# Optimization experiments

Measured on AMD Instinct MI355X. Metric: run time of the kernel, lower is better.

Reference implementation:

```python
import jax, jax.numpy as jnp
import numpy as np

_N = 2048          # matrix_size (A_sparse.shape[0] in the original)
_NNZ = 32768       # number of factor / pred entries
_LOGCOND_EPS = 1e-12


def setup_inputs() -> dict:
    key = jax.random.key(0)
    k1, k2, k3, k4, k5 = jax.random.split(key, 5)
    pred_values = jax.random.normal(k1, (_NNZ,), dtype=jnp.float32)
    active_scales = jax.random.uniform(k2, (_NNZ,), dtype=jnp.float32) * 0.05
    A_factor = jax.random.normal(k3, (_N, _N), dtype=jnp.float32)
    factor_rows = jax.random.randint(k4, (_NNZ,), 0, _N, dtype=jnp.int32)
    factor_cols = jax.random.randint(k5, (_NNZ,), 0, _N, dtype=jnp.int32)
    return {
        "pred_values": pred_values,
        "active_scales": active_scales,
        "A_factor": A_factor,
        "factor_rows": factor_rows,
        "factor_cols": factor_cols,
    }


def reference(pred_values, active_scales, A_factor, factor_rows, factor_cols):
    n = A_factor.shape[0]
    dt = pred_values.dtype
    # SPD system matrix A (stands in for the original fixed A_sparse)
    A = A_factor @ A_factor.T / jnp.asarray(n, dt) + jnp.eye(n, dtype=dt)
    # Sparse factor L assembled from predicted values (scatter-add, dup-safe),
    # unit diagonal keeps L A L^T well conditioned / SPD.
    L = jnp.eye(n, dtype=dt).at[factor_rows, factor_cols].add(pred_values * active_scales)
    # Preconditioned matrix M = L A L^T (symmetric PSD)
    M = L @ A @ L.T
    M = 0.5 * (M + M.T)
    evals = jnp.linalg.eigvalsh(M)  # ascending
    lam_min = jnp.maximum(evals[0], _LOGCOND_EPS)
    lam_max = jnp.maximum(evals[-1], _LOGCOND_EPS)
    # loss = log(lambda_max) - log(lambda_min) = log condition number
    return jnp.log(lam_max) - jnp.log(lam_min)
```

## Files before the change

kernel.cpp:

```cpp
#include <hip/hip_runtime.h>

#define N2 2048
#define NNZ 32768
#define LK 22
#define NBL 128
#define BINCAP 64

typedef __attribute__((ext_vector_type(8))) _Float16 half8;
typedef __attribute__((ext_vector_type(4))) float f32x4;

#define AGENT __HIP_MEMORY_SCOPE_AGENT
#define AS1C(p) ((const __attribute__((address_space(1))) unsigned int*)(p))
#define AS3(p)  ((__attribute__((address_space(3))) unsigned int*)(p))

__device__ __forceinline__ unsigned short f2h(float f) {
  _Float16 h = (_Float16)f;
  return *(unsigned short*)&h;
}
__device__ __forceinline__ float h2f(unsigned short u) {
  _Float16 h = *(_Float16*)&u;
  return (float)h;
}

__global__ __launch_bounds__(256) void convert_kernel(const float* __restrict__ W,
                                                      unsigned short* __restrict__ Hf,
                                                      unsigned* __restrict__ cnt) {
  if (blockIdx.x < 8) cnt[blockIdx.x * 256 + threadIdx.x] = 0;
  int i4 = blockIdx.x * 256 + threadIdx.x;
  float4 w = ((const float4*)W)[i4];
  ushort4 h;
  h.x = f2h(w.x); h.y = f2h(w.y); h.z = f2h(w.z); h.w = f2h(w.w);
  ((ushort4*)Hf)[i4] = h;
}

__device__ __forceinline__ void stage_tiles(const unsigned short* __restrict__ Hf,
                                            unsigned short* Xb, unsigned short* Yb,
                                            int row0, int col0, int kk,
                                            int srowX, int srowY, int scol, int wq) {
  __builtin_amdgcn_global_load_lds(
      AS1C(Hf + (size_t)(row0 + srowX) * 2048 + kk + scol),
      AS3(Xb + (wq * 16) * 32), 16, 0, 0);
#pragma unroll
  for (int q = 0; q < 2; ++q) {
    __builtin_amdgcn_global_load_lds(
        AS1C(Hf + (size_t)(col0 + srowY + q * 16) * 2048 + kk + scol),
        AS3(Yb + (wq * 32 + q * 16) * 32), 16, 0, 0);
  }
}

__global__ __launch_bounds__(512) void gemm_f16_kernel(const unsigned short* __restrict__ Hf,
                                                       unsigned short* __restrict__ Ah,
                                                       const float* __restrict__ pred,
                                                       const float* __restrict__ scal,
                                                       const int* __restrict__ rows,
                                                       const int* __restrict__ cols,
                                                       unsigned* __restrict__ cnt,
                                                       int* __restrict__ bcol,
                                                       float* __restrict__ bval) {
  const int tid = threadIdx.x;
  if (blockIdx.x < 64) {
    int k = blockIdx.x * 512 + tid;
    int r = rows[k];
    unsigned pos = atomicAdd(&cnt[r], 1u);
    if (pos < BINCAP) {
      bcol[r * BINCAP + pos] = cols[k];
      bval[r * BINCAP + pos] = pred[k] * scal[k];
    }
  }

  int bi, bj;
  bool diag;
  if (blockIdx.x < 32) {
    bi = blockIdx.x; bj = bi >> 1; diag = true;
  } else {
    int idx = blockIdx.x - 32;
    int j = 0;
    while (j < 14 && idx >= (j + 1) * (30 - j)) ++j;
    bj = j;
    bi = 2 * j + 2 + (idx - j * (31 - j));
    diag = false;
  }

  __shared__ __align__(16) char smem[49152];
  unsigned short* Xs = (unsigned short*)smem;
  unsigned short* Ys = (unsigned short*)(smem + 16384);
  float* Cred = (float*)smem;

  const int w = tid >> 6, lane = tid & 63;
  const int half = w >> 2, wq = w & 3;
  const int row0 = bi * 64, col0 = bj * 128;
  const int m0 = (wq & 1) * 32, n0 = (wq >> 1) * 64;
  f32x4 acc[2][4];
#pragma unroll
  for (int a = 0; a < 2; ++a)
#pragma unroll
    for (int b = 0; b < 4; ++b) acc[a][b] = (f32x4){0.f, 0.f, 0.f, 0.f};
  const int mrow = lane & 15, kseg = (lane >> 4) * 8;
  const int srowX = wq * 16 + (lane >> 2);
  const int srowY = wq * 32 + (lane >> 2);
  const int scol = (lane & 3) * 8;
  const int kbase = half * 1024;

  stage_tiles(Hf, Xs + (half * 2 + 0) * 2048, Ys + (half * 2 + 0) * 4096,
              row0, col0, kbase, srowX, srowY, scol, wq);

  for (int t = 0; t < 32; ++t) {
    const int cur = t & 1;
    __syncthreads();
    if (t < 31)
      stage_tiles(Hf, Xs + (half * 2 + (cur ^ 1)) * 2048,
                  Ys + (half * 2 + (cur ^ 1)) * 4096,
                  row0, col0, kbase + (t + 1) * 32, srowX, srowY, scol, wq);
    const unsigned short* Xb = Xs + (half * 2 + cur) * 2048;
    const unsigned short* Yb = Ys + (half * 2 + cur) * 4096;
    half8 af[2], bf[4];
#pragma unroll
    for (int q = 0; q < 2; ++q)
      af[q] = *(const half8*)(Xb + (m0 + q * 16 + mrow) * 32 + kseg);
#pragma unroll
    for (int q = 0; q < 4; ++q)
      bf[q] = *(const half8*)(Yb + (n0 + q * 16 + mrow) * 32 + kseg);
#pragma unroll
    for (int mt = 0; mt < 2; ++mt)
#pragma unroll
      for (int nt = 0; nt < 4; ++nt)
        acc[mt][nt] = __builtin_amdgcn_mfma_f32_16x16x32_f16(af[mt], bf[nt], acc[mt][nt], 0, 0, 0);
  }
  const int crow = (lane >> 4) * 4, ccol = lane & 15;
  __syncthreads();
  if (half == 1) {
#pragma unroll
    for (int mt = 0; mt < 2; ++mt)
#pragma unroll
      for (int nt = 0; nt < 4; ++nt)
#pragma unroll
        for (int r = 0; r < 4; ++r)
          Cred[(m0 + mt * 16 + crow + r) * 132 + n0 + nt * 16 + ccol] = acc[mt][nt][r];
  }
  __syncthreads();
  if (half == 0) {
    const float invn = 1.0f / 2048.0f;
#pragma unroll
    for (int mt = 0; mt < 2; ++mt)
#pragma unroll
      for (int nt = 0; nt < 4; ++nt) {
        const int gi0 = row0 + m0 + mt * 16 + crow;
        const int gj = col0 + n0 + nt * 16 + ccol;
        size_t base = (size_t)gi0 * 2048 + gj;
#pragma unroll
        for (int r = 0; r < 4; ++r) {
          const int li = (m0 + mt * 16 + crow + r) * 132 + n0 + nt * 16 + ccol;
          float val = (acc[mt][nt][r] + Cred[li]) * invn +
                      ((gi0 + r == gj) ? 1.0f : 0.0f);
          Ah[base + (size_t)r * 2048] = f2h(val);
          if (!diag) Cred[li] = val;
        }
      }
  }
  if (!diag) {
    __syncthreads();
    const int orow = tid >> 2;
    const int cseg = (tid & 3) * 16;
    unsigned short mv[16];
#pragma unroll
    for (int k = 0; k < 16; ++k)
      mv[k] = f2h(Cred[(cseg + k) * 132 + orow]);
    uint4* dst = (uint4*)(Ah + (size_t)(col0 + orow) * 2048 + row0 + cseg);
    dst[0] = *(uint4*)&mv[0];
    dst[1] = *(uint4*)&mv[8];
  }
}

__global__ __launch_bounds__(256) void gatherF_kernel(const unsigned* __restrict__ cnt,
                                                      const int* __restrict__ bcol,
                                                      const float* __restrict__ bval,
                                                      const unsigned short* __restrict__ Ah,
                                                      unsigned short* __restrict__ F) {
  const int r = blockIdx.x, tid = threadIdx.x;
  __shared__ int scol_[BINCAP];
  __shared__ float sval_[BINCAP];
  const unsigned ne = min(cnt[r], (unsigned)BINCAP);
  if (tid < ne) {
    scol_[tid] = bcol[r * BINCAP + tid];
    sval_[tid] = bval[r * BINCAP + tid];
  }
  __syncthreads();
  float acc[8] = {0.f, 0.f, 0.f, 0.f, 0.f, 0.f, 0.f, 0.f};
  unsigned e = 0;
  for (; e + 8 <= ne; e += 8) {
    uint4 q[8];
#pragma unroll
    for (int u = 0; u < 8; ++u)
      q[u] = *(const uint4*)(Ah + (size_t)scol_[e + u] * 2048 + tid * 8);
#pragma unroll
    for (int u = 0; u < 8; ++u) {
      half8 hv = *(half8*)&q[u];
      const float v = sval_[e + u];
#pragma unroll
      for (int k = 0; k < 8; ++k) acc[k] += v * (float)hv[k];
    }
  }
  for (; e + 4 <= ne; e += 4) {
    uint4 q[4];
#pragma unroll
    for (int u = 0; u < 4; ++u)
      q[u] = *(const uint4*)(Ah + (size_t)scol_[e + u] * 2048 + tid * 8);
#pragma unroll
    for (int u = 0; u < 4; ++u) {
      half8 hv = *(half8*)&q[u];
      const float v = sval_[e + u];
#pragma unroll
      for (int k = 0; k < 8; ++k) acc[k] += v * (float)hv[k];
    }
  }
  for (; e < ne; ++e) {
    uint4 qq = *(const uint4*)(Ah + (size_t)scol_[e] * 2048 + tid * 8);
    half8 hv = *(half8*)&qq;
    const float v = sval_[e];
#pragma unroll
    for (int k = 0; k < 8; ++k) acc[k] += v * (float)hv[k];
  }
  unsigned short o[8];
#pragma unroll
  for (int k = 0; k < 8; ++k) o[k] = f2h(acc[k]);
  *(uint4*)(F + (size_t)r * 2048 + tid * 8) = *(uint4*)o;
}

__global__ __launch_bounds__(256) void transpose_kernel(const unsigned short* __restrict__ F,
                                                        unsigned short* __restrict__ Ft) {
  __shared__ unsigned short T2[64][66];
  const int bi = blockIdx.x, bj = blockIdx.y;
  const int c8 = (threadIdx.x & 7) * 8;
  const int rr = threadIdx.x >> 3;
#pragma unroll
  for (int h = 0; h < 2; ++h) {
    const int r = rr + h * 32;
    uint4 raw = *(const uint4*)(F + (size_t)(bj * 64 + r) * 2048 + bi * 64 + c8);
    const unsigned* pw = (const unsigned*)&raw;
#pragma unroll
    for (int i = 0; i < 4; ++i)
      *(unsigned*)&T2[r][c8 + i * 2] = pw[i];
  }
  __syncthreads();
#pragma unroll
  for (int h = 0; h < 2; ++h) {
    const int r = rr + h * 32;
    unsigned short tv[8];
#pragma unroll
    for (int k = 0; k < 8; ++k) tv[k] = T2[c8 + k][r];
    *(uint4*)(Ft + (size_t)(bi * 64 + r) * 2048 + bj * 64 + c8) = *(uint4*)tv;
  }
}

__global__ __launch_bounds__(256) void finalM_kernel(const unsigned* __restrict__ cnt,
                                                     const int* __restrict__ bcol,
                                                     const float* __restrict__ bval,
                                                     const unsigned short* __restrict__ Ah,
                                                     const unsigned short* __restrict__ F,
                                                     const unsigned short* __restrict__ Ft,
                                                     float* __restrict__ M) {
  const int r = blockIdx.x, tid = threadIdx.x;
  __shared__ int scol_[BINCAP];
  __shared__ float sval_[BINCAP];
  const unsigned ne = min(cnt[r], (unsigned)BINCAP);
  if (tid < ne) {
    scol_[tid] = bcol[r * BINCAP + tid];
    sval_[tid] = bval[r * BINCAP + tid];
  }
  __syncthreads();
  float acc[8] = {0.f, 0.f, 0.f, 0.f, 0.f, 0.f, 0.f, 0.f};
  unsigned e = 0;
  for (; e + 8 <= ne; e += 8) {
    uint4 q[8];
#pragma unroll
    for (int u = 0; u < 8; ++u)
      q[u] = *(const uint4*)(Ft + (size_t)scol_[e + u] * 2048 + tid * 8);
#pragma unroll
    for (int u = 0; u < 8; ++u) {
      half8 hv = *(half8*)&q[u];
      const float v = sval_[e + u];
#pragma unroll
      for (int k = 0; k < 8; ++k) acc[k] += v * (float)hv[k];
    }
  }
  for (; e + 4 <= ne; e += 4) {
    uint4 q[4];
#pragma unroll
    for (int u = 0; u < 4; ++u)
      q[u] = *(const uint4*)(Ft + (size_t)scol_[e + u] * 2048 + tid * 8);
#pragma unroll
    for (int u = 0; u < 4; ++u) {
      half8 hv = *(half8*)&q[u];
      const float v = sval_[e + u];
#pragma unroll
      for (int k = 0; k < 8; ++k) acc[k] += v * (float)hv[k];
    }
  }
  for (; e < ne; ++e) {
    uint4 qq = *(const uint4*)(Ft + (size_t)scol_[e] * 2048 + tid * 8);
    half8 hv = *(half8*)&qq;
    const float v = sval_[e];
#pragma unroll
    for (int k = 0; k < 8; ++k) acc[k] += v * (float)hv[k];
  }
  const size_t off = (size_t)r * 2048 + tid * 8;
  uint4 ra = *(const uint4*)(Ah + off);
  uint4 rf = *(const uint4*)(F + off);
  uint4 rt = *(const uint4*)(Ft + off);
  half8 ha = *(half8*)&ra, hf = *(half8*)&rf, ht = *(half8*)&rt;
  float out[8];
#pragma unroll
  for (int k = 0; k < 8; ++k)
    out[k] = (float)ha[k] + ((float)hf[k] + (float)ht[k]) + acc[k];
  float4* Mo = (float4*)(M + off);
  Mo[0] = (float4){out[0], out[1], out[2], out[3]};
  Mo[1] = (float4){out[4], out[5], out[6], out[7]};
}

__device__ __forceinline__ float block_sum8(float v, float* red) {
#pragma unroll
  for (int off = 32; off; off >>= 1) v += __shfl_down(v, off);
  if ((threadIdx.x & 63) == 0) red[threadIdx.x >> 6] = v;
  __syncthreads();
  float r = ((red[0] + red[1]) + (red[2] + red[3])) +
            ((red[4] + red[5]) + (red[6] + red[7]));
  __syncthreads();
  return r;
}

__global__ __launch_bounds__(512) void lanczos_kernel(const float* __restrict__ M,
                                                      unsigned long long* __restrict__ Z0,
                                                      unsigned long long* __restrict__ Z1,
                                                      float* __restrict__ out) {
  const int tid = threadIdx.x, b = blockIdx.x;
  const int wave = tid >> 6, lane = tid & 63;
  __shared__ __align__(16) float Mlds[16 * 2048];
  __shared__ __align__(16) float VA[2048];
  __shared__ __align__(16) float VB[2048];
  __shared__ float red[8];
  __shared__ float al[LK + 2], b2[LK + 2];
  __shared__ float bnds[2], res[2];

  const float* Mblk = M + (size_t)b * 16 * 2048;
#pragma unroll
  for (int q = 0; q < 16; ++q)
    __builtin_amdgcn_global_load_lds(AS1C(Mblk + wave * 4096 + q * 256 + lane * 4),
                                     AS3(Mlds + wave * 4096 + q * 256), 16, 0, 0);

  float pv[4];
  float part = 0.f;
#pragma unroll
  for (int t = 0; t < 4; ++t) {
    int i = t * 512 + tid;
    unsigned u = (unsigned)i * 2654435761u;
    u ^= u >> 16; u *= 2246822519u; u ^= u >> 13;
    float rv = (float)(u >> 8) * (2.f / 16777216.f) - 1.f;
    pv[t] = rv;
    part += rv * rv;
  }
  float nrm = block_sum8(part, red);
  float innm = rsqrtf(nrm);
#pragma unroll
  for (int t = 0; t < 4; ++t) {
    int i = t * 512 + tid;
    VA[i] = pv[t] * innm;
    VB[i] = 0.f;
  }
  __syncthreads();

  float* Vcur = VA;
  float* Vprev = VB;
  float beta_prev = 0.f;

  for (int j = 1; j <= LK; ++j) {
    unsigned long long* Z = (j & 1) ? Z0 : Z1;
#pragma unroll
    for (int rr = 0; rr < 2; ++rr) {
      const int r = b * 16 + wave * 2 + rr;
      const float4* Mr = (const float4*)(Mlds + (wave * 2 + rr) * 2048);
      float s = 0.f;
#pragma unroll
      for (int t = 0; t < 8; ++t) {
        int idx = t * 64 + lane;
        float4 m4 = Mr[idx];
        float4 v4 = ((const float4*)Vcur)[idx];
        s += m4.x * v4.x + m4.y * v4.y + m4.z * v4.z + m4.w * v4.w;
      }
#pragma unroll
      for (int off = 32; off; off >>= 1) s += __shfl_down(s, off);
      if (lane == 0) {
        float zv = s - beta_prev * Vprev[r];
        unsigned long long pk = ((unsigned long long)(unsigned)j << 32) |
                                (unsigned long long)(unsigned)__float_as_uint(zv);
        __hip_atomic_store(&Z[r], pk, __ATOMIC_RELAXED, AGENT);
      }
    }

    float va[4];
#pragma unroll
    for (int t = 0; t < 4; ++t) va[t] = Vcur[t * 512 + tid];

    unsigned long long w4[4];
    int rounds = 0;
    for (;;) {
      bool ok = true;
#pragma unroll
      for (int t = 0; t < 4; ++t) {
        w4[t] = __hip_atomic_load(&Z[t * 512 + tid], __ATOMIC_RELAXED, AGENT);
        ok &= ((unsigned)(w4[t] >> 32) == (unsigned)j);
      }
      if (ok) break;
      if (rounds == 1)      __builtin_amdgcn_s_sleep(1);
      else if (rounds == 2) __builtin_amdgcn_s_sleep(2);
      else if (rounds >= 3) __builtin_amdgcn_s_sleep(8);
      ++rounds;
    }
    float za[4];
    float pa = 0.f;
#pragma unroll
    for (int t = 0; t < 4; ++t) {
      za[t] = __uint_as_float((unsigned)w4[t]);
      pa += za[t] * va[t];
    }
    float alpha = block_sum8(pa, red);
    float pb = 0.f;
#pragma unroll
    for (int t = 0; t < 4; ++t) {
      float rsd = za[t] - alpha * va[t];
      pb += rsd * rsd;
    }
    float beta2 = block_sum8(pb, red);
    float beta = sqrtf(fmaxf(beta2, 1e-30f));
    float invb = 1.f / beta;
    if (tid == 0) { al[j] = alpha; b2[j] = beta2; }
#pragma unroll
    for (int t = 0; t < 4; ++t) {
      int i = t * 512 + tid;
      Vprev[i] = (za[t] - alpha * va[t]) * invb;
    }
    float* tmp = Vprev; Vprev = Vcur; Vcur = tmp;
    beta_prev = beta;
    __syncthreads();
  }

  if (b == 0) {
    if (tid == 0) {
      float lo = 1e30f, hi = -1e30f;
      for (int i = 1; i <= LK; ++i) {
        float bl = (i > 1) ? sqrtf(b2[i - 1]) : 0.f;
        float br = (i < LK) ? sqrtf(b2[i]) : 0.f;
        lo = fminf(lo, al[i] - bl - br);
        hi = fmaxf(hi, al[i] + bl + br);
      }
      bnds[0] = lo; bnds[1] = hi;
    }
    __syncthreads();
    if (wave < 2) {
      const int tcount = (wave == 0) ? 1 : LK;
      float lo = bnds[0], hi = bnds[1];
      for (int round = 0; round < 4; ++round) {
        float x = lo + (hi - lo) * (float)(lane + 1) * (1.f / 65.f);
        int cnt = 0;
        float d = al[1] - x;
        if (fabsf(d) < 1e-25f) d = -1e-25f;
        if (d < 0.f) cnt++;
        for (int i = 2; i <= LK; ++i) {
          d = (al[i] - x) - b2[i - 1] / d;
          if (fabsf(d) < 1e-25f) d = -1e-25f;
          if (d < 0.f) cnt++;
        }
        bool ab = (cnt >= tcount);
        float cand_hi = ab ? x : hi;
        float cand_lo = ab ? lo : x;
#pragma unroll
        for (int off = 32; off; off >>= 1) {
          cand_hi = fminf(cand_hi, __shfl_down(cand_hi, off));
          cand_lo = fmaxf(cand_lo, __shfl_down(cand_lo, off));
        }
        cand_hi = __shfl(cand_hi, 0);
        cand_lo = __shfl(cand_lo, 0);
        hi = cand_hi;
        lo = fminf(cand_lo, hi);
      }
      if (lane == 0) res[wave] = 0.5f * (lo + hi);
    }
    __syncthreads();
    if (tid == 0) {
      float lmin = fmaxf(res[0], 1e-12f);
      float lmax = fmaxf(res[1], 1e-12f);
      out[0] = logf(lmax) - logf(lmin);
    }
  }
}

extern "C" void kernel_launch(void* const* d_in, const int* in_sizes, int n_in,
                              void* d_out, int out_size, void* d_ws, size_t ws_size,
                              hipStream_t stream) {
  const float* pred = (const float*)d_in[0];
  const float* scal = (const float*)d_in[1];
  const float* W    = (const float*)d_in[2];
  const int*   rows = (const int*)d_in[3];
  const int*   cols = (const int*)d_in[4];
  float* out = (float*)d_out;

  char* ws = (char*)d_ws;
  const size_t MB = 1024 * 1024;
  unsigned short* Hf = (unsigned short*)(ws);
  unsigned short* Ah = (unsigned short*)(ws + 8 * MB);
  unsigned short* F  = (unsigned short*)(ws + 16 * MB);
  unsigned short* Ft = (unsigned short*)(ws);
  float* M = (float*)(ws + 24 * MB);
  char* ctrl = ws + 40 * MB;
  unsigned* cnt  = (unsigned*)(ctrl);
  int*      bcol = (int*)(ctrl + 8192);
  float*    bval = (float*)(ctrl + 8192 + 524288);
  unsigned long long* Z0 = (unsigned long long*)(ctrl + 8192 + 1048576);
  unsigned long long* Z1 = (unsigned long long*)(ctrl + 8192 + 1048576 + 16384);

  convert_kernel<<<4096, 256, 0, stream>>>(W, Hf, cnt);
  gemm_f16_kernel<<<272, 512, 0, stream>>>(Hf, Ah, pred, scal, rows, cols, cnt, bcol, bval);

  gatherF_kernel<<<2048, 256, 0, stream>>>(cnt, bcol, bval, Ah, F);
  transpose_kernel<<<dim3(32, 32), 256, 0, stream>>>(F, Ft);
  finalM_kernel<<<2048, 256, 0, stream>>>(cnt, bcol, bval, Ah, F, Ft, M);

  lanczos_kernel<<<NBL, 512, 0, stream>>>(M, Z0, Z1, out);
}
```

Baseline: 251.2 us.

## Replace sparse row-gather products with dense fp16 MFMA GEMMs on scattered S

```diff
diff --git a/kernel.cpp b/kernel.cpp
--- a/kernel.cpp
+++ b/kernel.cpp
@@ -4,7 +4,6 @@
 #define NNZ 32768
 #define LK 22
 #define NBL 128
-#define BINCAP 64
 
 typedef __attribute__((ext_vector_type(8))) _Float16 half8;
 typedef __attribute__((ext_vector_type(4))) float f32x4;
@@ -24,27 +23,78 @@
 
 __global__ __launch_bounds__(256) void convert_kernel(const float* __restrict__ W,
                                                       unsigned short* __restrict__ Hf,
-                                                      unsigned* __restrict__ cnt) {
-  if (blockIdx.x < 8) cnt[blockIdx.x * 256 + threadIdx.x] = 0;
+                                                      float* __restrict__ Sf) {
   int i4 = blockIdx.x * 256 + threadIdx.x;
+  ((float4*)Sf)[i4] = (float4){0.f, 0.f, 0.f, 0.f};
   float4 w = ((const float4*)W)[i4];
   ushort4 h;
   h.x = f2h(w.x); h.y = f2h(w.y); h.z = f2h(w.z); h.w = f2h(w.w);
   ((ushort4*)Hf)[i4] = h;
 }
 
-__device__ __forceinline__ void stage_tiles(const unsigned short* __restrict__ Hf,
-                                            unsigned short* Xb, unsigned short* Yb,
-                                            int row0, int col0, int kk,
-                                            int srowX, int srowY, int scol, int wq) {
+__global__ __launch_bounds__(256) void cvtS_kernel(const float* __restrict__ Sf,
+                                                   unsigned short* __restrict__ Sh) {
+  int i4 = blockIdx.x * 256 + threadIdx.x;
+  float4 s = ((const float4*)Sf)[i4];
+  ushort4 h;
+  h.x = f2h(s.x); h.y = f2h(s.y); h.z = f2h(s.z); h.w = f2h(s.w);
+  ((ushort4*)Sh)[i4] = h;
+}
+
+__device__ __forceinline__ void stage_tiles2(const unsigned short* __restrict__ X,
+                                             const unsigned short* __restrict__ Y,
+                                             unsigned short* Xb, unsigned short* Yb,
+                                             int row0, int col0, int kk,
+                                             int srowX, int srowY, int scol, int wq) {
   __builtin_amdgcn_global_load_lds(
-      AS1C(Hf + (size_t)(row0 + srowX) * 2048 + kk + scol),
+      AS1C(X + (size_t)(row0 + srowX) * 2048 + kk + scol),
       AS3(Xb + (wq * 16) * 32), 16, 0, 0);
 #pragma unroll
   for (int q = 0; q < 2; ++q) {
     __builtin_amdgcn_global_load_lds(
-        AS1C(Hf + (size_t)(col0 + srowY + q * 16) * 2048 + kk + scol),
+        AS1C(Y + (size_t)(col0 + srowY + q * 16) * 2048 + kk + scol),
         AS3(Yb + (wq * 32 + q * 16) * 32), 16, 0, 0);
+  }
+}
+
+__device__ __forceinline__ void gemm_core(const unsigned short* __restrict__ X,
+                                          const unsigned short* __restrict__ Y,
+                                          char* smem, int tid, int row0, int col0,
+                                          f32x4 acc[2][4]) {
+  unsigned short* Xs = (unsigned short*)smem;
+  unsigned short* Ys = (unsigned short*)(smem + 16384);
+  const int w = tid >> 6, lane = tid & 63;
+  const int half = w >> 2, wq = w & 3;
+  const int m0 = (wq & 1) * 32, n0 = (wq >> 1) * 64;
+  const int mrow = lane & 15, kseg = (lane >> 4) * 8;
+  const int srowX = wq * 16 + (lane >> 2);
+  const int srowY = wq * 32 + (lane >> 2);
+  const int scol = (lane & 3) * 8;
+  const int kbase = half * 1024;
+
+  stage_tiles2(X, Y, Xs + (half * 2 + 0) * 2048, Ys + (half * 2 + 0) * 4096,
+               row0, col0, kbase, srowX, srowY, scol, wq);
+  for (int t = 0; t < 32; ++t) {
+    const int cur = t & 1;
+    __syncthreads();
+    if (t < 31)
+      stage_tiles2(X, Y, Xs + (half * 2 + (cur ^ 1)) * 2048,
+                   Ys + (half * 2 + (cur ^ 1)) * 4096,
+                   row0, col0, kbase + (t + 1) * 32, srowX, srowY, scol, wq);
+    const unsigned short* Xb = Xs + (half * 2 + cur) * 2048;
+    const unsigned short* Yb = Ys + (half * 2 + cur) * 4096;
+    half8 af[2], bf[4];
+#pragma unroll
+    for (int q = 0; q < 2; ++q)
+      af[q] = *(const half8*)(Xb + (m0 + q * 16 + mrow) * 32 + kseg);
+#pragma unroll
+    for (int q = 0; q < 4; ++q)
+      bf[q] = *(const half8*)(Yb + (n0 + q * 16 + mrow) * 32 + kseg);
+#pragma unroll
+    for (int mt = 0; mt < 2; ++mt)
+#pragma unroll
+      for (int nt = 0; nt < 4; ++nt)
+        acc[mt][nt] = __builtin_amdgcn_mfma_f32_16x16x32_f16(af[mt], bf[nt], acc[mt][nt], 0, 0, 0);
   }
 }
 
@@ -54,18 +104,11 @@
                                                        const float* __restrict__ scal,
                                                        const int* __restrict__ rows,
                                                        const int* __restrict__ cols,
-                                                       unsigned* __restrict__ cnt,
-                                                       int* __restrict__ bcol,
-                                                       float* __restrict__ bval) {
+                                                       float* __restrict__ Sf) {
   const int tid = threadIdx.x;
   if (blockIdx.x < 64) {
     int k = blockIdx.x * 512 + tid;
-    int r = rows[k];
-    unsigned pos = atomicAdd(&cnt[r], 1u);
-    if (pos < BINCAP) {
-      bcol[r * BINCAP + pos] = cols[k];
-      bval[r * BINCAP + pos] = pred[k] * scal[k];
-    }
+    atomicAdd(&Sf[(size_t)rows[k] * 2048 + cols[k]], pred[k] * scal[k]);
   }
 
   int bi, bj;
@@ -82,10 +125,7 @@
   }
 
   __shared__ __align__(16) char smem[49152];
-  unsigned short* Xs = (unsigned short*)smem;
-  unsigned short* Ys = (unsigned short*)(smem + 16384);
   float* Cred = (float*)smem;
-
   const int w = tid >> 6, lane = tid & 63;
   const int half = w >> 2, wq = w & 3;
   const int row0 = bi * 64, col0 = bj * 128;
@@ -95,37 +135,9 @@
   for (int a = 0; a < 2; ++a)
 #pragma unroll
     for (int b = 0; b < 4; ++b) acc[a][b] = (f32x4){0.f, 0.f, 0.f, 0.f};
-  const int mrow = lane & 15, kseg = (lane >> 4) * 8;
-  const int srowX = wq * 16 + (lane >> 2);
-  const int srowY = wq * 32 + (lane >> 2);
-  const int scol = (lane & 3) * 8;
-  const int kbase = half * 1024;
-
-  stage_tiles(Hf, Xs + (half * 2 + 0) * 2048, Ys + (half * 2 + 0) * 4096,
-              row0, col0, kbase, srowX, srowY, scol, wq);
-
-  for (int t = 0; t < 32; ++t) {
-    const int cur = t & 1;
-    __syncthreads();
-    if (t < 31)
-      stage_tiles(Hf, Xs + (half * 2 + (cur ^ 1)) * 2048,
-                  Ys + (half * 2 + (cur ^ 1)) * 4096,
-                  row0, col0, kbase + (t + 1) * 32, srowX, srowY, scol, wq);
-    const unsigned short* Xb = Xs + (half * 2 + cur) * 2048;
-    const unsigned short* Yb = Ys + (half * 2 + cur) * 4096;
-    half8 af[2], bf[4];
-#pragma unroll
-    for (int q = 0; q < 2; ++q)
-      af[q] = *(const half8*)(Xb + (m0 + q * 16 + mrow) * 32 + kseg);
-#pragma unroll
-    for (int q = 0; q < 4; ++q)
-      bf[q] = *(const half8*)(Yb + (n0 + q * 16 + mrow) * 32 + kseg);
-#pragma unroll
-    for (int mt = 0; mt < 2; ++mt)
-#pragma unroll
-      for (int nt = 0; nt < 4; ++nt)
-        acc[mt][nt] = __builtin_amdgcn_mfma_f32_16x16x32_f16(af[mt], bf[nt], acc[mt][nt], 0, 0, 0);
-  }
+
+  gemm_core(Hf, Hf, smem, tid, row0, col0, acc);
+
   const int crow = (lane >> 4) * 4, ccol = lane & 15;
   __syncthreads();
   if (half == 1) {
@@ -171,59 +183,52 @@
   }
 }
 
-__global__ __launch_bounds__(256) void gatherF_kernel(const unsigned* __restrict__ cnt,
-                                                      const int* __restrict__ bcol,
-                                                      const float* __restrict__ bval,
-                                                      const unsigned short* __restrict__ Ah,
-                                                      unsigned short* __restrict__ F) {
-  const int r = blockIdx.x, tid = threadIdx.x;
-  __shared__ int scol_[BINCAP];
-  __shared__ float sval_[BINCAP];
-  const unsigned ne = min(cnt[r], (unsigned)BINCAP);
-  if (tid < ne) {
-    scol_[tid] = bcol[r * BINCAP + tid];
-    sval_[tid] = bval[r * BINCAP + tid];
-  }
-  __syncthreads();
-  float acc[8] = {0.f, 0.f, 0.f, 0.f, 0.f, 0.f, 0.f, 0.f};
-  unsigned e = 0;
-  for (; e + 8 <= ne; e += 8) {
-    uint4 q[8];
-#pragma unroll
-    for (int u = 0; u < 8; ++u)
-      q[u] = *(const uint4*)(Ah + (size_t)scol_[e + u] * 2048 + tid * 8);
-#pragma unroll
-    for (int u = 0; u < 8; ++u) {
-      half8 hv = *(half8*)&q[u];
-      const float v = sval_[e + u];
-#pragma unroll
-      for (int k = 0; k < 8; ++k) acc[k] += v * (float)hv[k];
-    }
-  }
-  for (; e + 4 <= ne; e += 4) {
-    uint4 q[4];
-#pragma unroll
-    for (int u = 0; u < 4; ++u)
-      q[u] = *(const uint4*)(Ah + (size_t)scol_[e + u] * 2048 + tid * 8);
-#pragma unroll
-    for (int u = 0; u < 4; ++u) {
-      half8 hv = *(half8*)&q[u];
-      const float v = sval_[e + u];
-#pragma unroll
-      for (int k = 0; k < 8; ++k) acc[k] += v * (float)hv[k];
-    }
-  }
-  for (; e < ne; ++e) {
-    uint4 qq = *(const uint4*)(Ah + (size_t)scol_[e] * 2048 + tid * 8);
-    half8 hv = *(half8*)&qq;
-    const float v = sval_[e];
-#pragma unroll
-    for (int k = 0; k < 8; ++k) acc[k] += v * (float)hv[k];
-  }
-  unsigned short o[8];
-#pragma unroll
-  for (int k = 0; k < 8; ++k) o[k] = f2h(acc[k]);
-  *(uint4*)(F + (size_t)r * 2048 + tid * 8) = *(uint4*)o;
+__global__ __launch_bounds__(512) void gemmSA_kernel(const unsigned short* __restrict__ Sh,
+                                                     const unsigned short* __restrict__ Ah,
+                                                     unsigned short* __restrict__ F) {
+  const int tid = threadIdx.x;
+  const int bi = blockIdx.x >> 4, bj = blockIdx.x & 15;
+  __shared__ __align__(16) char smem[49152];
+  float* Cred = (float*)smem;
+  const int w = tid >> 6, lane = tid & 63;
+  const int half = w >> 2, wq = w & 3;
+  const int row0 = bi * 64, col0 = bj * 128;
+  const int m0 = (wq & 1) * 32, n0 = (wq >> 1) * 64;
+  f32x4 acc[2][4];
+#pragma unroll
+  for (int a = 0; a < 2; ++a)
+#pragma unroll
+    for (int b = 0; b < 4; ++b) acc[a][b] = (f32x4){0.f, 0.f, 0.f, 0.f};
+
+  gemm_core(Sh, Ah, smem, tid, row0, col0, acc);
+
+  const int crow = (lane >> 4) * 4, ccol = lane & 15;
+  __syncthreads();
+  if (half == 1) {
+#pragma unroll
+    for (int mt = 0; mt < 2; ++mt)
+#pragma unroll
+      for (int nt = 0; nt < 4; ++nt)
+#pragma unroll
+        for (int r = 0; r < 4; ++r)
+          Cred[(m0 + mt * 16 + crow + r) * 132 + n0 + nt * 16 + ccol] = acc[mt][nt][r];
+  }
+  __syncthreads();
+  if (half == 0) {
+#pragma unroll
+    for (int mt = 0; mt < 2; ++mt)
+#pragma unroll
+      for (int nt = 0; nt < 4; ++nt) {
+        const int gi0 = row0 + m0 + mt * 16 + crow;
+        const int gj = col0 + n0 + nt * 16 + ccol;
+        size_t base = (size_t)gi0 * 2048 + gj;
+#pragma unroll
+        for (int r = 0; r < 4; ++r) {
+          const int li = (m0 + mt * 16 + crow + r) * 132 + n0 + nt * 16 + ccol;
+          F[base + (size_t)r * 2048] = f2h(acc[mt][nt][r] + Cred[li]);
+        }
+      }
+  }
 }
 
 __global__ __launch_bounds__(256) void transpose_kernel(const unsigned short* __restrict__ F,
@@ -252,69 +257,56 @@
   }
 }
 
-__global__ __launch_bounds__(256) void finalM_kernel(const unsigned* __restrict__ cnt,
-                                                     const int* __restrict__ bcol,
-                                                     const float* __restrict__ bval,
+__global__ __launch_bounds__(512) void gemmSM_kernel(const unsigned short* __restrict__ Sh,
+                                                     const unsigned short* __restrict__ Fy,
                                                      const unsigned short* __restrict__ Ah,
-                                                     const unsigned short* __restrict__ F,
                                                      const unsigned short* __restrict__ Ft,
                                                      float* __restrict__ M) {
-  const int r = blockIdx.x, tid = threadIdx.x;
-  __shared__ int scol_[BINCAP];
-  __shared__ float sval_[BINCAP];
-  const unsigned ne = min(cnt[r], (unsigned)BINCAP);
-  if (tid < ne) {
-    scol_[tid] = bcol[r * BINCAP + tid];
-    sval_[tid] = bval[r * BINCAP + tid];
-  }
-  __syncthreads();
-  float acc[8] = {0.f, 0.f, 0.f, 0.f, 0.f, 0.f, 0.f, 0.f};
-  unsigned e = 0;
-  for (; e + 8 <= ne; e += 8) {
-    uint4 q[8];
-#pragma unroll
-    for (int u = 0; u < 8; ++u)
-      q[u] = *(const uint4*)(Ft + (size_t)scol_[e + u] * 2048 + tid * 8);
-#pragma unroll
-    for (int u = 0; u < 8; ++u) {
-      half8 hv = *(half8*)&q[u];
-      const float v = sval_[e + u];
-#pragma unroll
-      for (int k = 0; k < 8; ++k) acc[k] += v * (float)hv[k];
-    }
-  }
-  for (; e + 4 <= ne; e += 4) {
-    uint4 q[4];
-#pragma unroll
-    for (int u = 0; u < 4; ++u)
-      q[u] = *(const uint4*)(Ft + (size_t)scol_[e + u] * 2048 + tid * 8);
-#pragma unroll
-    for (int u = 0; u < 4; ++u) {
-      half8 hv = *(half8*)&q[u];
-      const float v = sval_[e + u];
-#pragma unroll
-      for (int k = 0; k < 8; ++k) acc[k] += v * (float)hv[k];
-    }
-  }
-  for (; e < ne; ++e) {
-    uint4 qq = *(const uint4*)(Ft + (size_t)scol_[e] * 2048 + tid * 8);
-    half8 hv = *(half8*)&qq;
-    const float v = sval_[e];
-#pragma unroll
-    for (int k = 0; k < 8; ++k) acc[k] += v * (float)hv[k];
-  }
-  const size_t off = (size_t)r * 2048 + tid * 8;
-  uint4 ra = *(const uint4*)(Ah + off);
-  uint4 rf = *(const uint4*)(F + off);
-  uint4 rt = *(const uint4*)(Ft + off);
-  half8 ha = *(half8*)&ra, hf = *(half8*)&rf, ht = *(half8*)&rt;
-  float out[8];
-#pragma unroll
-  for (int k = 0; k < 8; ++k)
-    out[k] = (float)ha[k] + ((float)hf[k] + (float)ht[k]) + acc[k];
-  float4* Mo = (float4*)(M + off);
-  Mo[0] = (float4){out[0], out[1], out[2], out[3]};
-  Mo[1] = (float4){out[4], out[5], out[6], out[7]};
+  const int tid = threadIdx.x;
+  const int bi = blockIdx.x >> 4, bj = blockIdx.x & 15;
+  __shared__ __align__(16) char smem[49152];
+  float* Cred = (float*)smem;
+  const int w = tid >> 6, lane = tid & 63;
+  const int half = w >> 2, wq = w & 3;
+  const int row0 = bi * 64, col0 = bj * 128;
+  const int m0 = (wq & 1) * 32, n0 = (wq >> 1) * 64;
+  f32x4 acc[2][4];
+#pragma unroll
+  for (int a = 0; a < 2; ++a)
+#pragma unroll
+    for (int b = 0; b < 4; ++b) acc[a][b] = (f32x4){0.f, 0.f, 0.f, 0.f};
+
+  gemm_core(Sh, Fy, smem, tid, row0, col0, acc);
+
+  const int crow = (lane >> 4) * 4, ccol = lane & 15;
+  __syncthreads();
+  if (half == 1) {
+#pragma unroll
+    for (int mt = 0; mt < 2; ++mt)
+#pragma unroll
+      for (int nt = 0; nt < 4; ++nt)
+#pragma unroll
+        for (int r = 0; r < 4; ++r)
+          Cred[(m0 + mt * 16 + crow + r) * 132 + n0 + nt * 16 + ccol] = acc[mt][nt][r];
+  }
+  __syncthreads();
+  if (half == 0) {
+#pragma unroll
+    for (int mt = 0; mt < 2; ++mt)
+#pragma unroll
+      for (int nt = 0; nt < 4; ++nt) {
+        const int gi0 = row0 + m0 + mt * 16 + crow;
+        const int gj = col0 + n0 + nt * 16 + ccol;
+        size_t base = (size_t)gi0 * 2048 + gj;
+#pragma unroll
+        for (int r = 0; r < 4; ++r) {
+          const size_t off = base + (size_t)r * 2048;
+          const int li = (m0 + mt * 16 + crow + r) * 132 + n0 + nt * 16 + ccol;
+          float sft = acc[mt][nt][r] + Cred[li];
+          M[off] = h2f(Ah[off]) + (h2f(Fy[off]) + h2f(Ft[off])) + sft;
+        }
+      }
+  }
 }
 
 __device__ __forceinline__ float block_sum8(float v, float* red) {
@@ -506,23 +498,21 @@
   char* ws = (char*)d_ws;
   const size_t MB = 1024 * 1024;
   unsigned short* Hf = (unsigned short*)(ws);
+  unsigned short* Sh = (unsigned short*)(ws);
   unsigned short* Ah = (unsigned short*)(ws + 8 * MB);
   unsigned short* F  = (unsigned short*)(ws + 16 * MB);
-  unsigned short* Ft = (unsigned short*)(ws);
-  float* M = (float*)(ws + 24 * MB);
-  char* ctrl = ws + 40 * MB;
-  unsigned* cnt  = (unsigned*)(ctrl);
-  int*      bcol = (int*)(ctrl + 8192);
-  float*    bval = (float*)(ctrl + 8192 + 524288);
-  unsigned long long* Z0 = (unsigned long long*)(ctrl + 8192 + 1048576);
-  unsigned long long* Z1 = (unsigned long long*)(ctrl + 8192 + 1048576 + 16384);
-
-  convert_kernel<<<4096, 256, 0, stream>>>(W, Hf, cnt);
-  gemm_f16_kernel<<<272, 512, 0, stream>>>(Hf, Ah, pred, scal, rows, cols, cnt, bcol, bval);
-
-  gatherF_kernel<<<2048, 256, 0, stream>>>(cnt, bcol, bval, Ah, F);
+  float* Sf = (float*)(ws + 24 * MB);
+  float* M  = (float*)(ws + 24 * MB);
+  unsigned short* Ft = (unsigned short*)(ws + 40 * MB);
+  unsigned long long* Z0 = (unsigned long long*)(ws + 48 * MB);
+  unsigned long long* Z1 = (unsigned long long*)(ws + 48 * MB + 16384);
+
+  convert_kernel<<<4096, 256, 0, stream>>>(W, Hf, Sf);
+  gemm_f16_kernel<<<272, 512, 0, stream>>>(Hf, Ah, pred, scal, rows, cols, Sf);
+  cvtS_kernel<<<4096, 256, 0, stream>>>(Sf, Sh);
+  gemmSA_kernel<<<512, 512, 0, stream>>>(Sh, Ah, F);
   transpose_kernel<<<dim3(32, 32), 256, 0, stream>>>(F, Ft);
-  finalM_kernel<<<2048, 256, 0, stream>>>(cnt, bcol, bval, Ah, F, Ft, M);
+  gemmSM_kernel<<<512, 512, 0, stream>>>(Sh, F, Ah, Ft, M);
 
   lanczos_kernel<<<NBL, 512, 0, stream>>>(M, Z0, Z1, out);
 }
```

Result: slower. 284.5 us (+13.3%).

## Rewrite L A L^T as (LW)(LW)^T/n plus sparse L L^T

Applied to the files above, without the earlier changes.

```diff
diff --git a/kernel.cpp b/kernel.cpp
--- a/kernel.cpp
+++ b/kernel.cpp
@@ -22,10 +22,13 @@
   return (float)h;
 }
 
+
 __global__ __launch_bounds__(256) void convert_kernel(const float* __restrict__ W,
                                                       unsigned short* __restrict__ Hf,
-                                                      unsigned* __restrict__ cnt) {
-  if (blockIdx.x < 8) cnt[blockIdx.x * 256 + threadIdx.x] = 0;
+                                                      unsigned* __restrict__ cntR,
+                                                      unsigned* __restrict__ cntC) {
+  if (blockIdx.x < 8)       cntR[blockIdx.x * 256 + threadIdx.x] = 0;
+  else if (blockIdx.x < 16) cntC[(blockIdx.x - 8) * 256 + threadIdx.x] = 0;
   int i4 = blockIdx.x * 256 + threadIdx.x;
   float4 w = ((const float4*)W)[i4];
   ushort4 h;
@@ -33,41 +36,102 @@
   ((ushort4*)Hf)[i4] = h;
 }
 
-__device__ __forceinline__ void stage_tiles(const unsigned short* __restrict__ Hf,
-                                            unsigned short* Xb, unsigned short* Yb,
-                                            int row0, int col0, int kk,
-                                            int srowX, int srowY, int scol, int wq) {
+__global__ __launch_bounds__(256) void fill_kernel(const float* __restrict__ pred,
+                                                   const float* __restrict__ scal,
+                                                   const int* __restrict__ rows,
+                                                   const int* __restrict__ cols,
+                                                   unsigned* __restrict__ cntR,
+                                                   int* __restrict__ binRc,
+                                                   float* __restrict__ binRv,
+                                                   unsigned* __restrict__ cntC,
+                                                   int* __restrict__ binCr,
+                                                   float* __restrict__ binCv) {
+  int k = blockIdx.x * 256 + threadIdx.x;
+  int r = rows[k], c = cols[k];
+  float v = pred[k] * scal[k];
+  unsigned pR = atomicAdd(&cntR[r], 1u);
+  if (pR < BINCAP) { binRc[r * BINCAP + pR] = c; binRv[r * BINCAP + pR] = v; }
+  unsigned pC = atomicAdd(&cntC[c], 1u);
+  if (pC < BINCAP) { binCr[c * BINCAP + pC] = r; binCv[c * BINCAP + pC] = v; }
+}
+
+__global__ __launch_bounds__(256) void gatherG_kernel(const unsigned* __restrict__ cntR,
+                                                      const int* __restrict__ binRc,
+                                                      const float* __restrict__ binRv,
+                                                      const unsigned short* __restrict__ Hf,
+                                                      unsigned short* __restrict__ Gh) {
+  const int r = blockIdx.x, tid = threadIdx.x;
+  __shared__ int scol_[BINCAP];
+  __shared__ float sval_[BINCAP];
+  const unsigned ne = min(cntR[r], (unsigned)BINCAP);
+  if (tid < ne) {
+    scol_[tid] = binRc[r * BINCAP + tid];
+    sval_[tid] = binRv[r * BINCAP + tid];
+  }
+  __syncthreads();
+  uint4 own = *(const uint4*)(Hf + (size_t)r * 2048 + tid * 8);
+  half8 ho = *(half8*)&own;
+  float acc[8];
+#pragma unroll
+  for (int k = 0; k < 8; ++k) acc[k] = (float)ho[k];
+  unsigned e = 0;
+  for (; e + 8 <= ne; e += 8) {
+    uint4 q[8];
+#pragma unroll
+    for (int u = 0; u < 8; ++u)
+      q[u] = *(const uint4*)(Hf + (size_t)scol_[e + u] * 2048 + tid * 8);
+#pragma unroll
+    for (int u = 0; u < 8; ++u) {
+      half8 hv = *(half8*)&q[u];
+      const float v = sval_[e + u];
+#pragma unroll
+      for (int k = 0; k < 8; ++k) acc[k] += v * (float)hv[k];
+    }
+  }
+  for (; e + 4 <= ne; e += 4) {
+    uint4 q[4];
+#pragma unroll
+    for (int u = 0; u < 4; ++u)
+      q[u] = *(const uint4*)(Hf + (size_t)scol_[e + u] * 2048 + tid * 8);
+#pragma unroll
+    for (int u = 0; u < 4; ++u) {
+      half8 hv = *(half8*)&q[u];
+      const float v = sval_[e + u];
+#pragma unroll
+      for (int k = 0; k < 8; ++k) acc[k] += v * (float)hv[k];
+    }
+  }
+  for (; e < ne; ++e) {
+    uint4 qq = *(const uint4*)(Hf + (size_t)scol_[e] * 2048 + tid * 8);
+    half8 hv = *(half8*)&qq;
+    const float v = sval_[e];
+#pragma unroll
+    for (int k = 0; k < 8; ++k) acc[k] += v * (float)hv[k];
+  }
+  unsigned short o[8];
+#pragma unroll
+  for (int k = 0; k < 8; ++k) o[k] = f2h(acc[k]);
+  *(uint4*)(Gh + (size_t)r * 2048 + tid * 8) = *(uint4*)o;
+}
+
+__device__ __forceinline__ void stage_tiles2(const unsigned short* __restrict__ X,
+                                             unsigned short* Xb, unsigned short* Yb,
+                                             int row0, int col0, int kk,
+                                             int srowX, int srowY, int scol, int wq) {
   __builtin_amdgcn_global_load_lds(
-      AS1C(Hf + (size_t)(row0 + srowX) * 2048 + kk + scol),
+      AS1C(X + (size_t)(row0 + srowX) * 2048 + kk + scol),
       AS3(Xb + (wq * 16) * 32), 16, 0, 0);
 #pragma unroll
   for (int q = 0; q < 2; ++q) {
     __builtin_amdgcn_global_load_lds(
-        AS1C(Hf + (size_t)(col0 + srowY + q * 16) * 2048 + kk + scol),
+        AS1C(X + (size_t)(col0 + srowY + q * 16) * 2048 + kk + scol),
         AS3(Yb + (wq * 32 + q * 16) * 32), 16, 0, 0);
   }
 }
 
-__global__ __launch_bounds__(512) void gemm_f16_kernel(const unsigned short* __restrict__ Hf,
-                                                       unsigned short* __restrict__ Ah,
-                                                       const float* __restrict__ pred,
-                                                       const float* __restrict__ scal,
-                                                       const int* __restrict__ rows,
-                                                       const int* __restrict__ cols,
-                                                       unsigned* __restrict__ cnt,
-                                                       int* __restrict__ bcol,
-                                                       float* __restrict__ bval) {
+__global__ __launch_bounds__(512) void gemmM_kernel(const unsigned short* __restrict__ Gh,
+                                                    float* __restrict__ M) {
   const int tid = threadIdx.x;
-  if (blockIdx.x < 64) {
-    int k = blockIdx.x * 512 + tid;
-    int r = rows[k];
-    unsigned pos = atomicAdd(&cnt[r], 1u);
-    if (pos < BINCAP) {
-      bcol[r * BINCAP + pos] = cols[k];
-      bval[r * BINCAP + pos] = pred[k] * scal[k];
-    }
-  }
-
   int bi, bj;
   bool diag;
   if (blockIdx.x < 32) {
@@ -101,16 +165,15 @@
   const int scol = (lane & 3) * 8;
   const int kbase = half * 1024;
 
-  stage_tiles(Hf, Xs + (half * 2 + 0) * 2048, Ys + (half * 2 + 0) * 4096,
-              row0, col0, kbase, srowX, srowY, scol, wq);
-
+  stage_tiles2(Gh, Xs + (half * 2 + 0) * 2048, Ys + (half * 2 + 0) * 4096,
+               row0, col0, kbase, srowX, srowY, scol, wq);
   for (int t = 0; t < 32; ++t) {
     const int cur = t & 1;
     __syncthreads();
     if (t < 31)
-      stage_tiles(Hf, Xs + (half * 2 + (cur ^ 1)) * 2048,
-                  Ys + (half * 2 + (cur ^ 1)) * 4096,
-                  row0, col0, kbase + (t + 1) * 32, srowX, srowY, scol, wq);
+      stage_tiles2(Gh, Xs + (half * 2 + (cur ^ 1)) * 2048,
+                   Ys + (half * 2 + (cur ^ 1)) * 4096,
+                   row0, col0, kbase + (t + 1) * 32, srowX, srowY, scol, wq);
     const unsigned short* Xb = Xs + (half * 2 + cur) * 2048;
     const unsigned short* Yb = Ys + (half * 2 + cur) * 4096;
     half8 af[2], bf[4];
@@ -152,7 +215,7 @@
           const int li = (m0 + mt * 16 + crow + r) * 132 + n0 + nt * 16 + ccol;
           float val = (acc[mt][nt][r] + Cred[li]) * invn +
                       ((gi0 + r == gj) ? 1.0f : 0.0f);
-          Ah[base + (size_t)r * 2048] = f2h(val);
+          M[base + (size_t)r * 2048] = val;
           if (!diag) Cred[li] = val;
         }
       }
@@ -161,160 +224,49 @@
     __syncthreads();
     const int orow = tid >> 2;
     const int cseg = (tid & 3) * 16;
-    unsigned short mv[16];
+    float mv[16];
 #pragma unroll
     for (int k = 0; k < 16; ++k)
-      mv[k] = f2h(Cred[(cseg + k) * 132 + orow]);
-    uint4* dst = (uint4*)(Ah + (size_t)(col0 + orow) * 2048 + row0 + cseg);
-    dst[0] = *(uint4*)&mv[0];
-    dst[1] = *(uint4*)&mv[8];
-  }
-}
-
-__global__ __launch_bounds__(256) void gatherF_kernel(const unsigned* __restrict__ cnt,
-                                                      const int* __restrict__ bcol,
-                                                      const float* __restrict__ bval,
-                                                      const unsigned short* __restrict__ Ah,
-                                                      unsigned short* __restrict__ F) {
-  const int r = blockIdx.x, tid = threadIdx.x;
-  __shared__ int scol_[BINCAP];
-  __shared__ float sval_[BINCAP];
-  const unsigned ne = min(cnt[r], (unsigned)BINCAP);
-  if (tid < ne) {
-    scol_[tid] = bcol[r * BINCAP + tid];
-    sval_[tid] = bval[r * BINCAP + tid];
-  }
-  __syncthreads();
-  float acc[8] = {0.f, 0.f, 0.f, 0.f, 0.f, 0.f, 0.f, 0.f};
-  unsigned e = 0;
-  for (; e + 8 <= ne; e += 8) {
-    uint4 q[8];
-#pragma unroll
-    for (int u = 0; u < 8; ++u)
-      q[u] = *(const uint4*)(Ah + (size_t)scol_[e + u] * 2048 + tid * 8);
-#pragma unroll
-    for (int u = 0; u < 8; ++u) {
-      half8 hv = *(half8*)&q[u];
-      const float v = sval_[e + u];
-#pragma unroll
-      for (int k = 0; k < 8; ++k) acc[k] += v * (float)hv[k];
-    }
-  }
-  for (; e + 4 <= ne; e += 4) {
-    uint4 q[4];
-#pragma unroll
-    for (int u = 0; u < 4; ++u)
-      q[u] = *(const uint4*)(Ah + (size_t)scol_[e + u] * 2048 + tid * 8);
-#pragma unroll
-    for (int u = 0; u < 4; ++u) {
-      half8 hv = *(half8*)&q[u];
-      const float v = sval_[e + u];
-#pragma unroll
-      for (int k = 0; k < 8; ++k) acc[k] += v * (float)hv[k];
-    }
-  }
-  for (; e < ne; ++e) {
-    uint4 qq = *(const uint4*)(Ah + (size_t)scol_[e] * 2048 + tid * 8);
-    half8 hv = *(half8*)&qq;
-    const float v = sval_[e];
-#pragma unroll
-    for (int k = 0; k < 8; ++k) acc[k] += v * (float)hv[k];
-  }
-  unsigned short o[8];
-#pragma unroll
-  for (int k = 0; k < 8; ++k) o[k] = f2h(acc[k]);
-  *(uint4*)(F + (size_t)r * 2048 + tid * 8) = *(uint4*)o;
-}
-
-__global__ __launch_bounds__(256) void transpose_kernel(const unsigned short* __restrict__ F,
-                                                        unsigned short* __restrict__ Ft) {
-  __shared__ unsigned short T2[64][66];
-  const int bi = blockIdx.x, bj = blockIdx.y;
-  const int c8 = (threadIdx.x & 7) * 8;
-  const int rr = threadIdx.x >> 3;
-#pragma unroll
-  for (int h = 0; h < 2; ++h) {
-    const int r = rr + h * 32;
-    uint4 raw = *(const uint4*)(F + (size_t)(bj * 64 + r) * 2048 + bi * 64 + c8);
-    const unsigned* pw = (const unsigned*)&raw;
-#pragma unroll
-    for (int i = 0; i < 4; ++i)
-      *(unsigned*)&T2[r][c8 + i * 2] = pw[i];
-  }
-  __syncthreads();
-#pragma unroll
-  for (int h = 0; h < 2; ++h) {
-    const int r = rr + h * 32;
-    unsigned short tv[8];
-#pragma unroll
-    for (int k = 0; k < 8; ++k) tv[k] = T2[c8 + k][r];
-    *(uint4*)(Ft + (size_t)(bi * 64 + r) * 2048 + bj * 64 + c8) = *(uint4*)tv;
-  }
-}
-
-__global__ __launch_bounds__(256) void finalM_kernel(const unsigned* __restrict__ cnt,
-                                                     const int* __restrict__ bcol,
-                                                     const float* __restrict__ bval,
-                                                     const unsigned short* __restrict__ Ah,
-                                                     const unsigned short* __restrict__ F,
-                                                     const unsigned short* __restrict__ Ft,
-                                                     float* __restrict__ M) {
-  const int r = blockIdx.x, tid = threadIdx.x;
-  __shared__ int scol_[BINCAP];
-  __shared__ float sval_[BINCAP];
-  const unsigned ne = min(cnt[r], (unsigned)BINCAP);
-  if (tid < ne) {
-    scol_[tid] = bcol[r * BINCAP + tid];
-    sval_[tid] = bval[r * BINCAP + tid];
-  }
-  __syncthreads();
-  float acc[8] = {0.f, 0.f, 0.f, 0.f, 0.f, 0.f, 0.f, 0.f};
-  unsigned e = 0;
-  for (; e + 8 <= ne; e += 8) {
-    uint4 q[8];
-#pragma unroll
-    for (int u = 0; u < 8; ++u)
-      q[u] = *(const uint4*)(Ft + (size_t)scol_[e + u] * 2048 + tid * 8);
-#pragma unroll
-    for (int u = 0; u < 8; ++u) {
-      half8 hv = *(half8*)&q[u];
-      const float v = sval_[e + u];
-#pragma unroll
-      for (int k = 0; k < 8; ++k) acc[k] += v * (float)hv[k];
-    }
-  }
-  for (; e + 4 <= ne; e += 4) {
-    uint4 q[4];
-#pragma unroll
-    for (int u = 0; u < 4; ++u)
-      q[u] = *(const uint4*)(Ft + (size_t)scol_[e + u] * 2048 + tid * 8);
-#pragma unroll
-    for (int u = 0; u < 4; ++u) {
-      half8 hv = *(half8*)&q[u];
-      const float v = sval_[e + u];
-#pragma unroll
-      for (int k = 0; k < 8; ++k) acc[k] += v * (float)hv[k];
-    }
-  }
-  for (; e < ne; ++e) {
-    uint4 qq = *(const uint4*)(Ft + (size_t)scol_[e] * 2048 + tid * 8);
-    half8 hv = *(half8*)&qq;
-    const float v = sval_[e];
-#pragma unroll
-    for (int k = 0; k < 8; ++k) acc[k] += v * (float)hv[k];
-  }
-  const size_t off = (size_t)r * 2048 + tid * 8;
-  uint4 ra = *(const uint4*)(Ah + off);
-  uint4 rf = *(const uint4*)(F + off);
-  uint4 rt = *(const uint4*)(Ft + off);
-  half8 ha = *(half8*)&ra, hf = *(half8*)&rf, ht = *(half8*)&rt;
-  float out[8];
-#pragma unroll
-  for (int k = 0; k < 8; ++k)
-    out[k] = (float)ha[k] + ((float)hf[k] + (float)ht[k]) + acc[k];
-  float4* Mo = (float4*)(M + off);
-  Mo[0] = (float4){out[0], out[1], out[2], out[3]};
-  Mo[1] = (float4){out[4], out[5], out[6], out[7]};
+      mv[k] = Cred[(cseg + k) * 132 + orow];
+    float4* dst = (float4*)(M + (size_t)(col0 + orow) * 2048 + row0 + cseg);
+    dst[0] = (float4){mv[0], mv[1], mv[2], mv[3]};
+    dst[1] = (float4){mv[4], mv[5], mv[6], mv[7]};
+    dst[2] = (float4){mv[8], mv[9], mv[10], mv[11]};
+    dst[3] = (float4){mv[12], mv[13], mv[14], mv[15]};
+  }
+}
+
+__global__ __launch_bounds__(256) void scatterS_kernel(const float* __restrict__ pred,
+                                                       const float* __restrict__ scal,
+                                                       const int* __restrict__ rows,
+                                                       const int* __restrict__ cols,
+                                                       const unsigned* __restrict__ cntC,
+                                                       const int* __restrict__ binCr,
+                                                       const float* __restrict__ binCv,
+                                                       float* __restrict__ M) {
+  const int tid = threadIdx.x;
+  if (blockIdx.x < 128) {
+    int k = blockIdx.x * 256 + tid;
+    int r = rows[k], c = cols[k];
+    float v = pred[k] * scal[k];
+    atomicAdd(&M[(size_t)r * 2048 + c], v);
+    atomicAdd(&M[(size_t)c * 2048 + r], v);
+    return;
+  }
+  const int c = blockIdx.x - 128;
+  __shared__ int rr_[BINCAP];
+  __shared__ float vv_[BINCAP];
+  const unsigned nc = min(cntC[c], (unsigned)BINCAP);
+  if (tid < nc) {
+    rr_[tid] = binCr[c * BINCAP + tid];
+    vv_[tid] = binCv[c * BINCAP + tid];
+  }
+  __syncthreads();
+  const unsigned np = nc * nc;
+  for (unsigned p = tid; p < np; p += 256) {
+    unsigned i1 = p / nc, i2 = p - i1 * nc;
+    atomicAdd(&M[(size_t)rr_[i1] * 2048 + rr_[i2]], vv_[i1] * vv_[i2]);
+  }
 }
 
 __device__ __forceinline__ float block_sum8(float v, float* red) {
@@ -506,23 +458,25 @@
   char* ws = (char*)d_ws;
   const size_t MB = 1024 * 1024;
   unsigned short* Hf = (unsigned short*)(ws);
-  unsigned short* Ah = (unsigned short*)(ws + 8 * MB);
-  unsigned short* F  = (unsigned short*)(ws + 16 * MB);
-  unsigned short* Ft = (unsigned short*)(ws);
-  float* M = (float*)(ws + 24 * MB);
-  char* ctrl = ws + 40 * MB;
-  unsigned* cnt  = (unsigned*)(ctrl);
-  int*      bcol = (int*)(ctrl + 8192);
-  float*    bval = (float*)(ctrl + 8192 + 524288);
-  unsigned long long* Z0 = (unsigned long long*)(ctrl + 8192 + 1048576);
-  unsigned long long* Z1 = (unsigned long long*)(ctrl + 8192 + 1048576 + 16384);
-
-  convert_kernel<<<4096, 256, 0, stream>>>(W, Hf, cnt);
-  gemm_f16_kernel<<<272, 512, 0, stream>>>(Hf, Ah, pred, scal, rows, cols, cnt, bcol, bval);
-
-  gatherF_kernel<<<2048, 256, 0, stream>>>(cnt, bcol, bval, Ah, F);
-  transpose_kernel<<<dim3(32, 32), 256, 0, stream>>>(F, Ft);
-  finalM_kernel<<<2048, 256, 0, stream>>>(cnt, bcol, bval, Ah, F, Ft, M);
+  unsigned short* Gh = (unsigned short*)(ws + 8 * MB);
+  float* M = (float*)(ws + 16 * MB);
+  char* ctrl = ws + 32 * MB;
+  unsigned* cntR = (unsigned*)(ctrl);
+  unsigned* cntC = (unsigned*)(ctrl + 8192);
+  int*      binRc = (int*)(ctrl + 16384);
+  float*    binRv = (float*)(ctrl + 16384 + 524288);
+  int*      binCr = (int*)(ctrl + 16384 + 2 * 524288);
+  float*    binCv = (float*)(ctrl + 16384 + 3 * 524288);
+  unsigned long long* Z0 = (unsigned long long*)(ctrl + 16384 + 4 * 524288);
+  unsigned long long* Z1 = (unsigned long long*)(ctrl + 16384 + 4 * 524288 + 16384);
+
+  convert_kernel<<<4096, 256, 0, stream>>>(W, Hf, cntR, cntC);
+  fill_kernel<<<NNZ / 256, 256, 0, stream>>>(pred, scal, rows, cols,
+                                             cntR, binRc, binRv, cntC, binCr, binCv);
+  gatherG_kernel<<<2048, 256, 0, stream>>>(cntR, binRc, binRv, Hf, Gh);
+  gemmM_kernel<<<272, 512, 0, stream>>>(Gh, M);
+  scatterS_kernel<<<2176, 256, 0, stream>>>(pred, scal, rows, cols,
+                                            cntC, binCr, binCv, M);
 
   lanczos_kernel<<<NBL, 512, 0, stream>>>(M, Z0, Z1, out);
 }
```

New measurement: 267.3 us. 6.4% more time.
